# Kernel optimization log

Hardware: AMD Instinct MI355X
Metric: run time of the kernel (lower is better)

The kernel has to match this reference:

```python
import jax, jax.numpy as jnp
import numpy as np

NUM_EMBEDDINGS = 8192
EMBEDDING_DIM = 256
COMMITMENT_COST = 0.25


def setup_inputs() -> dict:
    key = jax.random.key(0)
    kz, kw = jax.random.split(key)
    z = jax.random.normal(kz, (65536, EMBEDDING_DIM), dtype=jnp.float32)
    # nn.Embedding init: uniform(-1/K, 1/K)
    W = jax.random.uniform(kw, (NUM_EMBEDDINGS, EMBEDDING_DIM), dtype=jnp.float32,
                           minval=-1.0 / NUM_EMBEDDINGS, maxval=1.0 / NUM_EMBEDDINGS)
    return {"z": z, "W": W}


def reference(z, W):
    # distances[n, k] = ||z_n||^2 + ||W_k||^2 - 2 z_n . W_k  -> [N, K]
    distances = (jnp.sum(z * z, axis=1, keepdims=True)
                 + jnp.sum(W * W, axis=1)
                 - 2.0 * jnp.matmul(z, W.T))
    encoding_indices = jnp.argmin(distances, axis=1)  # [N]
    # one-hot @ W is just a gather of codebook rows
    quantized = W[encoding_indices]  # [N, D]
    e_latent_loss = jnp.mean((jax.lax.stop_gradient(quantized) - z) ** 2)
    q_latent_loss = jnp.mean((quantized - jax.lax.stop_gradient(z)) ** 2)
    loss = q_latent_loss + COMMITMENT_COST * e_latent_loss
    # straight-through estimator
    quantized_st = z + jax.lax.stop_gradient(quantized - z)
    return quantized_st, loss, encoding_indices[:, None]
```

## Files before the change

kernel.cpp:

```cpp
#include <hip/hip_runtime.h>

#define N_ROWS 65536
#define K_CODES 8192
#define DIM 256
#define CAP 56

#define LOSS_OFF (N_ROWS * DIM)
#define IDX_OFF (LOSS_OFF + 1)
#define OUT_WBF_U16 0
#define OUT_ZBF_U16 2097152
#define OUT_CAND_F 9437184

#define WS_LOSS 0
#define WS_ZNORM 64
#define WS_WNORM (WS_ZNORM + N_ROWS)
#define WS_MARGIN (WS_WNORM + K_CODES)
#define WS_CUT0 (WS_MARGIN + N_ROWS)
#define WS_CNT (WS_CUT0 + N_ROWS)
#define WS_OVF (WS_CNT + N_ROWS)
#define WS_OVFLIST (WS_OVF + 1)
#define WS_SLOT (((WS_OVFLIST + N_ROWS) + 1) & ~1)

typedef __bf16 bf16x8 __attribute__((ext_vector_type(8)));
typedef float f32x4 __attribute__((ext_vector_type(4)));


__device__ __forceinline__ float mul_rn_nofma(float a, float b) {
  float r;
  asm("v_mul_f32 %0, %1, %2" : "=v"(r) : "v"(a), "v"(b));
  return r;
}

__device__ __forceinline__ unsigned int f2bf(float f) {
  unsigned int u = __float_as_uint(f);
  return (u + 0x7FFFu + ((u >> 16) & 1u)) >> 16;
}

__device__ float dot_chain(const float* __restrict__ zp, const float* __restrict__ wp) {
  float acc = 0.0f;
#pragma unroll 8
  for (int d4 = 0; d4 < 64; ++d4) {
    const float4 a = *(const float4*)(zp + d4 * 4);
    const float4 b = *(const float4*)(wp + d4 * 4);
    acc = fmaf(a.x, b.x, acc);
    acc = fmaf(a.y, b.y, acc);
    acc = fmaf(a.z, b.z, acc);
    acc = fmaf(a.w, b.w, acc);
  }
  return acc;
}

__device__ __forceinline__ void glds16(const void* g, void* l) {
  __builtin_amdgcn_global_load_lds(
      (const __attribute__((address_space(1))) void*)(unsigned long long)(size_t)g,
      (__attribute__((address_space(3))) void*)(unsigned int)(size_t)l, 16, 0, 0);
}


__global__ void precvt_kernel(const float* __restrict__ z, const float* __restrict__ W,
                              unsigned short* __restrict__ outu) {
  const int t = blockIdx.x * blockDim.x + threadIdx.x;
  const int WQ = (K_CODES * DIM) / 4;
  const float4 v = (t < WQ) ? ((const float4*)W)[t] : ((const float4*)z)[t - WQ];
  uint2 p;
  p.x = f2bf(v.x) | (f2bf(v.y) << 16);
  p.y = f2bf(v.z) | (f2bf(v.w) << 16);
  ((uint2*)outu)[t] = p;
}

__global__ void norms_kernel(const float* __restrict__ z, const float* __restrict__ W,
                             float* __restrict__ ws) {
  const int tid = threadIdx.x;
  const int l = tid & 63, w = tid >> 6;
  const int j = l & 7, b = (l >> 3) & 1, rw = l >> 4;
  const int row = blockIdx.x * 16 + w * 4 + rw;
  const float* src = (row < N_ROWS) ? (z + (size_t)row * DIM + b * 128)
                                    : (W + (size_t)(row - N_ROWS) * DIM + b * 128);
  float a0 = src[j];
  float r = mul_rn_nofma(a0, a0);
  float s = fabsf(a0);
  for (int i = 8; i < 128; i += 8) {
    const float v = src[i + j];
    r = r + mul_rn_nofma(v, v);
    s = s + fabsf(v);
  }
  r = r + __shfl_xor(r, 1, 64);
  r = r + __shfl_xor(r, 2, 64);
  r = r + __shfl_xor(r, 4, 64);
  r = r + __shfl_xor(r, 8, 64);
  s = s + __shfl_xor(s, 1, 64);
  s = s + __shfl_xor(s, 2, 64);
  s = s + __shfl_xor(s, 4, 64);
  s = s + __shfl_xor(s, 8, 64);
  if ((l & 15) == 0) {
    if (row < N_ROWS) {
      ws[WS_ZNORM + row] = r;
      const float margin = 2.0e-6f * s + 4.0e-5f;
      ws[WS_MARGIN + row] = margin;
      ws[WS_CUT0 + row] = 3.10f * sqrtf(r) * 7.0467e-5f - margin;
      ((unsigned int*)ws)[WS_CNT + row] = 0u;
    } else {
      ws[WS_WNORM + (row - N_ROWS)] = r;
    }
  }
  if (blockIdx.x == 0 && tid == 0) {
    ws[WS_LOSS] = 0.0f;
    ((unsigned int*)ws)[WS_OVF] = 0u;
  }
}

__global__ __launch_bounds__(256) void gemm_screen_kernel(
    const unsigned short* __restrict__ zbf, const unsigned short* __restrict__ wbf,
    float* __restrict__ ws, uint2* __restrict__ candp) {
  __shared__ __align__(16) unsigned short As[2][128][32];
  __shared__ __align__(16) unsigned short Bs[2][128][32];
  __shared__ float cutbuf[128];

  const int tid = threadIdx.x;
  const int w = tid >> 6, l = tid & 63;
  const int lr = l & 15, lq = l >> 4;
  const int wr = (w >> 1) * 64, wc = (w & 1) * 64;
  const int rowBase = blockIdx.y * 128, colBase = blockIdx.x * 128;
  const int r16 = l >> 2, slot = l & 3;

  unsigned int* cntp = (unsigned int*)ws + WS_CNT;

  if (tid < 128) cutbuf[tid] = ws[WS_CUT0 + rowBase + tid];

  f32x4 acc[4][4];
#pragma unroll
  for (int mi = 0; mi < 4; ++mi)
#pragma unroll
    for (int ni = 0; ni < 4; ++ni) acc[mi][ni] = (f32x4){0.f, 0.f, 0.f, 0.f};

  auto STAGE = [&](int c, int b) {
#pragma unroll
    for (int j = 0; j < 2; ++j) {
      const int r_l = w * 32 + j * 16 + r16;
      const int ga = slot ^ (r_l & 3);
      glds16(zbf + (size_t)(rowBase + r_l) * DIM + c * 32 + ga * 8,
             &As[b][w * 32 + j * 16][0]);
      glds16(wbf + (size_t)(colBase + r_l) * DIM + c * 32 + ga * 8,
             &Bs[b][w * 32 + j * 16][0]);
    }
  };

  auto COMPUTE = [&](int b) {
    bf16x8 af[4], bfr[4];
#pragma unroll
    for (int mi = 0; mi < 4; ++mi) {
      const int r_l = wr + mi * 16 + lr;
      af[mi] = *(const bf16x8*)&As[b][r_l][(lq ^ (r_l & 3)) * 8];
    }
#pragma unroll
    for (int ni = 0; ni < 4; ++ni) {
      const int r_l = wc + ni * 16 + lr;
      bfr[ni] = *(const bf16x8*)&Bs[b][r_l][(lq ^ (r_l & 3)) * 8];
    }
#pragma unroll
    for (int mi = 0; mi < 4; ++mi)
#pragma unroll
      for (int ni = 0; ni < 4; ++ni)
        acc[mi][ni] =
            __builtin_amdgcn_mfma_f32_16x16x32_bf16(af[mi], bfr[ni], acc[mi][ni], 0, 0, 0);
  };

  STAGE(0, 0);
  __syncthreads();
#pragma unroll
  for (int c = 0; c < 8; ++c) {
    if (c < 7) STAGE(c + 1, (c + 1) & 1);
    COMPUTE(c & 1);
    __syncthreads();
  }

#pragma unroll
  for (int mi = 0; mi < 4; ++mi)
#pragma unroll
    for (int r = 0; r < 4; ++r) {
      const int lrow = wr + mi * 16 + lq * 4 + r;
      const float cut = cutbuf[lrow];
#pragma unroll
      for (int ni = 0; ni < 4; ++ni) {
        if (acc[mi][ni][r] >= cut) {
          const int grow = rowBase + lrow;
          const int gcol = colBase + wc + ni * 16 + lr;
          const unsigned int pos = atomicAdd(&cntp[grow], 1u);
          if (pos < CAP) {
            uint2 e;
            e.x = __float_as_uint(acc[mi][ni][r]);
            e.y = (unsigned int)gcol;
            candp[(size_t)grow * CAP + pos] = e;
          }
        }
      }
    }
}

__global__ void recheck_kernel(const float* __restrict__ z, const float* __restrict__ W,
                               float* __restrict__ ws, const uint2* __restrict__ candp,
                               float* __restrict__ out) {
  const int lane = threadIdx.x & 63;
  const int row = blockIdx.x * 4 + (threadIdx.x >> 6);
  const unsigned int cv = ((const unsigned int*)ws)[WS_CNT + row];
  const float margin = ws[WS_MARGIN + row];
  const float cut0 = ws[WS_CUT0 + row];
  bool fb = (cv == 0u) || (cv > CAP);
  uint2 e;
  e.x = 0u; e.y = 0u;
  float av = -3.4e38f;
  if (!fb && lane < (int)cv) {
    e = candp[(size_t)row * CAP + lane];
    av = __uint_as_float(e.x);
  }
  float candmax = av;
#pragma unroll
  for (int s = 1; s < 64; s <<= 1) candmax = fmaxf(candmax, __shfl_xor(candmax, s, 64));
  if (!fb && candmax - margin < cut0) fb = true;
  if (fb) {
    if (lane == 0) {
      ((unsigned long long*)((unsigned int*)ws + WS_SLOT))[row] = ~0ull;
      const unsigned int p = atomicAdd(&((unsigned int*)ws)[WS_OVF], 1u);
      ((unsigned int*)ws)[WS_OVFLIST + p] = (unsigned int)row;
    }
    return;
  }
  const float fcut = candmax - margin;
  unsigned long long key = ~0ull;
  if (lane < (int)cv && av >= fcut) {
    const int k = (int)e.y;
    const float zn = ws[WS_ZNORM + row];
    const float m = dot_chain(z + (size_t)row * DIM, W + (size_t)k * DIM);
    const float dist = (zn + ws[WS_WNORM + k]) - 2.0f * m;
    key = ((unsigned long long)__float_as_uint(dist) << 32) | (unsigned int)k;
  }
#pragma unroll
  for (int s = 1; s < 64; s <<= 1) {
    const unsigned long long o = (unsigned long long)__shfl_xor((long long)key, s, 64);
    key = (o < key) ? o : key;
  }
  if (lane == 0) out[IDX_OFF + row] = (float)(unsigned int)(key & 0xffffffffull);
}

__global__ void fallback_compute(const float* __restrict__ z, const float* __restrict__ W,
                                 float* __restrict__ ws) {
  __shared__ unsigned long long part[4];
  const unsigned int n = ((const unsigned int*)ws)[WS_OVF];
  unsigned long long* slots = (unsigned long long*)((unsigned int*)ws + WS_SLOT);
  const unsigned int total = n * 32u;
  for (unsigned int item = blockIdx.x; item < total; item += gridDim.x) {
    const int row = (int)((const unsigned int*)ws)[WS_OVFLIST + (item >> 5)];
    const int k = (int)(item & 31u) * 256 + threadIdx.x;
    const float zn = ws[WS_ZNORM + row];
    const float m = dot_chain(z + (size_t)row * DIM, W + (size_t)k * DIM);
    const float dist = (zn + ws[WS_WNORM + k]) - 2.0f * m;
    unsigned long long key =
        ((unsigned long long)__float_as_uint(dist) << 32) | (unsigned int)k;
#pragma unroll
    for (int s = 1; s < 64; s <<= 1) {
      const unsigned long long o = __shfl_xor((long long)key, s, 64);
      key = (o < key) ? o : key;
    }
    if ((threadIdx.x & 63) == 0) part[threadIdx.x >> 6] = key;
    __syncthreads();
    if (threadIdx.x == 0) {
      unsigned long long b = part[0];
      b = (part[1] < b) ? part[1] : b;
      b = (part[2] < b) ? part[2] : b;
      b = (part[3] < b) ? part[3] : b;
      atomicMin(&slots[row], b);
    }
    __syncthreads();
  }
}

__global__ void fallback_write(const float* __restrict__ ws, float* __restrict__ out) {
  const unsigned int i = blockIdx.x * blockDim.x + threadIdx.x;
  const unsigned int n = ((const unsigned int*)ws)[WS_OVF];
  if (i < n) {
    const int row = (int)((const unsigned int*)ws)[WS_OVFLIST + i];
    const unsigned long long key =
        ((const unsigned long long*)((const unsigned int*)ws + WS_SLOT))[row];
    out[IDX_OFF + row] = (float)(unsigned int)(key & 0xffffffffull);
  }
}

__global__ void gather_loss_kernel(const float* __restrict__ z, const float* __restrict__ W,
                                   float* __restrict__ out, float* __restrict__ ws) {
  const int tid = threadIdx.x;
  const int rowBase = blockIdx.x * 64;
  float lsum = 0.0f;
  for (int p = 0; p < 16; ++p) {
    const int row = rowBase + p * 4 + (tid >> 6);
    const int c4 = tid & 63;
    const int idx = (int)out[IDX_OFF + row];
    const float4 zv = *(const float4*)(z + (size_t)row * DIM + c4 * 4);
    const float4 qv = *(const float4*)(W + (size_t)idx * DIM + c4 * 4);
    float4 t, o;
    t.x = qv.x - zv.x; t.y = qv.y - zv.y; t.z = qv.z - zv.z; t.w = qv.w - zv.w;
    o.x = zv.x + t.x;  o.y = zv.y + t.y;  o.z = zv.z + t.z;  o.w = zv.w + t.w;
    *(float4*)(out + (size_t)row * DIM + c4 * 4) = o;
    lsum += t.x * t.x + t.y * t.y + t.z * t.z + t.w * t.w;
  }
#pragma unroll
  for (int m = 1; m < 64; m <<= 1) lsum += __shfl_xor(lsum, m, 64);
  __shared__ float part[4];
  if ((tid & 63) == 0) part[tid >> 6] = lsum;
  __syncthreads();
  if (tid == 0) atomicAdd(&ws[WS_LOSS], (part[0] + part[1]) + (part[2] + part[3]));
}

__global__ void finalize_kernel(const float* __restrict__ ws, float* __restrict__ out) {
  if (threadIdx.x == 0 && blockIdx.x == 0) {
    const float mean = ws[WS_LOSS] / (float)(N_ROWS * DIM);
    out[LOSS_OFF] = mean + 0.25f * mean;
  }
}

extern "C" void kernel_launch(void* const* d_in, const int* in_sizes, int n_in,
                              void* d_out, int out_size, void* d_ws, size_t ws_size,
                              hipStream_t stream) {
  (void)in_sizes; (void)n_in; (void)out_size; (void)ws_size;
  const float* z = (const float*)d_in[0];
  const float* W = (const float*)d_in[1];
  float* out = (float*)d_out;
  float* ws = (float*)d_ws;
  unsigned short* outu = (unsigned short*)d_out;
  const unsigned short* wbf = outu + OUT_WBF_U16;
  const unsigned short* zbf = outu + OUT_ZBF_U16;
  uint2* candp = (uint2*)((float*)d_out + OUT_CAND_F);

  hipLaunchKernelGGL(precvt_kernel, dim3(18432), dim3(256), 0, stream, z, W, outu);
  hipLaunchKernelGGL(norms_kernel, dim3((N_ROWS + K_CODES) / 16), dim3(256), 0, stream,
                     z, W, ws);
  hipLaunchKernelGGL(gemm_screen_kernel, dim3(K_CODES / 128, N_ROWS / 128), dim3(256),
                     0, stream, zbf, wbf, ws, candp);
  hipLaunchKernelGGL(recheck_kernel, dim3(N_ROWS / 4), dim3(256), 0, stream,
                     z, W, ws, candp, out);
  hipLaunchKernelGGL(fallback_compute, dim3(2048), dim3(256), 0, stream, z, W, ws);
  hipLaunchKernelGGL(fallback_write, dim3(256), dim3(256), 0, stream, ws, out);
  hipLaunchKernelGGL(gather_loss_kernel, dim3(N_ROWS / 64), dim3(256), 0, stream,
                     z, W, out, ws);
  hipLaunchKernelGGL(finalize_kernel, dim3(1), dim3(64), 0, stream, ws, out);
}
```

Before: 994.4 us.

## Fuse prep kernels, triple-buffer GEMM staging, swizzle blocks, drop fallback_write launch

Merges the bf16 conversion into the norms kernel so z and W are read once. The screening GEMM moves from double to triple-buffered LDS staging with explicit vmcnt waits, raw barriers and MFMA priority hints. It also uses a 1D grid with an XCD-aware block swizzle and a simpler swizzle for the LDS chunks. The fallback_write kernel is removed: fallback rows are marked -1 and resolved inside the gather kernel. This cuts launches and redundant traffic, at the cost of more LDS per block and fragile hand-tuned wait counts.

```diff
diff --git a/kernel.cpp b/kernel.cpp
--- a/kernel.cpp
+++ b/kernel.cpp
@@ -57,30 +57,24 @@
 }
 
 
-__global__ void precvt_kernel(const float* __restrict__ z, const float* __restrict__ W,
-                              unsigned short* __restrict__ outu) {
-  const int t = blockIdx.x * blockDim.x + threadIdx.x;
-  const int WQ = (K_CODES * DIM) / 4;
-  const float4 v = (t < WQ) ? ((const float4*)W)[t] : ((const float4*)z)[t - WQ];
-  uint2 p;
-  p.x = f2bf(v.x) | (f2bf(v.y) << 16);
-  p.y = f2bf(v.z) | (f2bf(v.w) << 16);
-  ((uint2*)outu)[t] = p;
-}
-
-__global__ void norms_kernel(const float* __restrict__ z, const float* __restrict__ W,
-                             float* __restrict__ ws) {
+__global__ void prep_kernel(const float* __restrict__ z, const float* __restrict__ W,
+                            float* __restrict__ ws, unsigned short* __restrict__ outu) {
   const int tid = threadIdx.x;
   const int l = tid & 63, w = tid >> 6;
   const int j = l & 7, b = (l >> 3) & 1, rw = l >> 4;
   const int row = blockIdx.x * 16 + w * 4 + rw;
-  const float* src = (row < N_ROWS) ? (z + (size_t)row * DIM + b * 128)
-                                    : (W + (size_t)(row - N_ROWS) * DIM + b * 128);
+  const bool isz = (row < N_ROWS);
+  const float* src = isz ? (z + (size_t)row * DIM + b * 128)
+                         : (W + (size_t)(row - N_ROWS) * DIM + b * 128);
+  unsigned short* dst = isz ? (outu + OUT_ZBF_U16 + (size_t)row * DIM + b * 128)
+                            : (outu + OUT_WBF_U16 + (size_t)(row - N_ROWS) * DIM + b * 128);
   float a0 = src[j];
+  dst[j] = (unsigned short)f2bf(a0);
   float r = mul_rn_nofma(a0, a0);
   float s = fabsf(a0);
   for (int i = 8; i < 128; i += 8) {
     const float v = src[i + j];
+    dst[i + j] = (unsigned short)f2bf(v);
     r = r + mul_rn_nofma(v, v);
     s = s + fabsf(v);
   }
@@ -93,7 +87,7 @@
   s = s + __shfl_xor(s, 4, 64);
   s = s + __shfl_xor(s, 8, 64);
   if ((l & 15) == 0) {
-    if (row < N_ROWS) {
+    if (isz) {
       ws[WS_ZNORM + row] = r;
       const float margin = 2.0e-6f * s + 4.0e-5f;
       ws[WS_MARGIN + row] = margin;
@@ -112,16 +106,18 @@
 __global__ __launch_bounds__(256) void gemm_screen_kernel(
     const unsigned short* __restrict__ zbf, const unsigned short* __restrict__ wbf,
     float* __restrict__ ws, uint2* __restrict__ candp) {
-  __shared__ __align__(16) unsigned short As[2][128][32];
-  __shared__ __align__(16) unsigned short Bs[2][128][32];
+  __shared__ __align__(16) unsigned short As[3][128][32];
+  __shared__ __align__(16) unsigned short Bs[3][128][32];
   __shared__ float cutbuf[128];
 
   const int tid = threadIdx.x;
   const int w = tid >> 6, l = tid & 63;
   const int lr = l & 15, lq = l >> 4;
   const int wr = (w >> 1) * 64, wc = (w & 1) * 64;
-  const int rowBase = blockIdx.y * 128, colBase = blockIdx.x * 128;
-  const int r16 = l >> 2, slot = l & 3;
+
+  const int bid = blockIdx.x;
+  const int swz = (bid & 7) * 4096 + (bid >> 3);
+  const int rowBase = (swz >> 6) * 128, colBase = (swz & 63) * 128;
 
   unsigned int* cntp = (unsigned int*)ws + WS_CNT;
 
@@ -133,11 +129,11 @@
 #pragma unroll
     for (int ni = 0; ni < 4; ++ni) acc[mi][ni] = (f32x4){0.f, 0.f, 0.f, 0.f};
 
+  const int ga = (l & 3) ^ ((l >> 3) & 3);
   auto STAGE = [&](int c, int b) {
 #pragma unroll
     for (int j = 0; j < 2; ++j) {
-      const int r_l = w * 32 + j * 16 + r16;
-      const int ga = slot ^ (r_l & 3);
+      const int r_l = w * 32 + j * 16 + (l >> 2);
       glds16(zbf + (size_t)(rowBase + r_l) * DIM + c * 32 + ga * 8,
              &As[b][w * 32 + j * 16][0]);
       glds16(wbf + (size_t)(colBase + r_l) * DIM + c * 32 + ga * 8,
@@ -147,31 +143,39 @@
 
   auto COMPUTE = [&](int b) {
     bf16x8 af[4], bfr[4];
-#pragma unroll
-    for (int mi = 0; mi < 4; ++mi) {
-      const int r_l = wr + mi * 16 + lr;
-      af[mi] = *(const bf16x8*)&As[b][r_l][(lq ^ (r_l & 3)) * 8];
-    }
-#pragma unroll
-    for (int ni = 0; ni < 4; ++ni) {
-      const int r_l = wc + ni * 16 + lr;
-      bfr[ni] = *(const bf16x8*)&Bs[b][r_l][(lq ^ (r_l & 3)) * 8];
-    }
+    const int ch = (lq ^ ((lr >> 1) & 3)) * 8;
+#pragma unroll
+    for (int mi = 0; mi < 4; ++mi) af[mi] = *(const bf16x8*)&As[b][wr + mi * 16 + lr][ch];
+#pragma unroll
+    for (int ni = 0; ni < 4; ++ni) bfr[ni] = *(const bf16x8*)&Bs[b][wc + ni * 16 + lr][ch];
+    __builtin_amdgcn_s_setprio(1);
 #pragma unroll
     for (int mi = 0; mi < 4; ++mi)
 #pragma unroll
       for (int ni = 0; ni < 4; ++ni)
         acc[mi][ni] =
             __builtin_amdgcn_mfma_f32_16x16x32_bf16(af[mi], bfr[ni], acc[mi][ni], 0, 0, 0);
+    __builtin_amdgcn_s_setprio(0);
   };
 
   STAGE(0, 0);
-  __syncthreads();
+  STAGE(1, 1);
+  STAGE(2, 2);
 #pragma unroll
   for (int c = 0; c < 8; ++c) {
-    if (c < 7) STAGE(c + 1, (c + 1) & 1);
-    COMPUTE(c & 1);
-    __syncthreads();
+    if (c < 6)
+      asm volatile("s_waitcnt vmcnt(8)" ::: "memory");
+    else if (c == 6)
+      asm volatile("s_waitcnt vmcnt(4)" ::: "memory");
+    else
+      asm volatile("s_waitcnt vmcnt(0)" ::: "memory");
+    __builtin_amdgcn_sched_barrier(0);
+    __builtin_amdgcn_s_barrier();
+    __builtin_amdgcn_sched_barrier(0);
+    COMPUTE(c % 3);
+    __builtin_amdgcn_sched_barrier(0);
+    __builtin_amdgcn_s_barrier();
+    if (c < 5) STAGE(c + 3, c % 3);
   }
 
 #pragma unroll
@@ -222,6 +226,7 @@
       ((unsigned long long*)((unsigned int*)ws + WS_SLOT))[row] = ~0ull;
       const unsigned int p = atomicAdd(&((unsigned int*)ws)[WS_OVF], 1u);
       ((unsigned int*)ws)[WS_OVFLIST + p] = (unsigned int)row;
+      out[IDX_OFF + row] = -1.0f;
     }
     return;
   }
@@ -274,17 +279,6 @@
   }
 }
 
-__global__ void fallback_write(const float* __restrict__ ws, float* __restrict__ out) {
-  const unsigned int i = blockIdx.x * blockDim.x + threadIdx.x;
-  const unsigned int n = ((const unsigned int*)ws)[WS_OVF];
-  if (i < n) {
-    const int row = (int)((const unsigned int*)ws)[WS_OVFLIST + i];
-    const unsigned long long key =
-        ((const unsigned long long*)((const unsigned int*)ws + WS_SLOT))[row];
-    out[IDX_OFF + row] = (float)(unsigned int)(key & 0xffffffffull);
-  }
-}
-
 __global__ void gather_loss_kernel(const float* __restrict__ z, const float* __restrict__ W,
                                    float* __restrict__ out, float* __restrict__ ws) {
   const int tid = threadIdx.x;
@@ -293,7 +287,13 @@
   for (int p = 0; p < 16; ++p) {
     const int row = rowBase + p * 4 + (tid >> 6);
     const int c4 = tid & 63;
-    const int idx = (int)out[IDX_OFF + row];
+    int idx = (int)out[IDX_OFF + row];
+    if (idx < 0) {
+      const unsigned long long key =
+          ((const unsigned long long*)((const unsigned int*)ws + WS_SLOT))[row];
+      idx = (int)(unsigned int)(key & 0xffffffffull);
+      out[IDX_OFF + row] = (float)idx;
+    }
     const float4 zv = *(const float4*)(z + (size_t)row * DIM + c4 * 4);
     const float4 qv = *(const float4*)(W + (size_t)idx * DIM + c4 * 4);
     float4 t, o;
@@ -330,15 +330,13 @@
   const unsigned short* zbf = outu + OUT_ZBF_U16;
   uint2* candp = (uint2*)((float*)d_out + OUT_CAND_F);
 
-  hipLaunchKernelGGL(precvt_kernel, dim3(18432), dim3(256), 0, stream, z, W, outu);
-  hipLaunchKernelGGL(norms_kernel, dim3((N_ROWS + K_CODES) / 16), dim3(256), 0, stream,
-                     z, W, ws);
-  hipLaunchKernelGGL(gemm_screen_kernel, dim3(K_CODES / 128, N_ROWS / 128), dim3(256),
-                     0, stream, zbf, wbf, ws, candp);
+  hipLaunchKernelGGL(prep_kernel, dim3((N_ROWS + K_CODES) / 16), dim3(256), 0, stream,
+                     z, W, ws, outu);
+  hipLaunchKernelGGL(gemm_screen_kernel, dim3((K_CODES / 128) * (N_ROWS / 128)),
+                     dim3(256), 0, stream, zbf, wbf, ws, candp);
   hipLaunchKernelGGL(recheck_kernel, dim3(N_ROWS / 4), dim3(256), 0, stream,
                      z, W, ws, candp, out);
   hipLaunchKernelGGL(fallback_compute, dim3(2048), dim3(256), 0, stream, z, W, ws);
-  hipLaunchKernelGGL(fallback_write, dim3(256), dim3(256), 0, stream, ws, out);
   hipLaunchKernelGGL(gather_loss_kernel, dim3(N_ROWS / 64), dim3(256), 0, stream,
                      z, W, out, ws);
   hipLaunchKernelGGL(finalize_kernel, dim3(1), dim3(64), 0, stream, ws, out);
```

Measured after the change: 1.469 ms. 1.48x slower.
